# Kernel tuning notes

Hardware: AMD Instinct MI355X
Metric: run time of the kernel (lower is better)

Reference implementation:

```python
import jax, jax.numpy as jnp
import numpy as np
from jax import lax

ALPHA = 0.2
BETA = 10.0
HALF = 1
ITERS = 10


def _slrelu(x):
    return ALPHA * x + (1.0 - ALPHA) * jax.nn.softplus(BETA * x) / BETA


def _std_kernel(sigma):
    # sigma: [C,1,1] -> per-channel L1-normalized Gaussian [C,1,K,K]
    C = sigma.shape[0]
    k = 2 * HALF + 1
    xs = jnp.arange(-HALF, HALF + 1, dtype=jnp.float32)
    r2 = xs[None, :] ** 2 + xs[:, None] ** 2            # [K,K]
    s = jnp.clip(sigma.reshape(C, 1, 1, 1), 1e-6, None)  # [C,1,1,1]
    ker = jnp.exp(-r2[None, None] / (2.0 * s ** 2))      # [C,1,K,K]
    return ker / (jnp.sum(ker, axis=(2, 3), keepdims=True) + 1e-12)


def _dwconv(x, ker):
    # depthwise conv, NCHW input, OIHW kernel [C,1,K,K], groups=C
    C = ker.shape[0]
    return lax.conv_general_dilated(
        x, ker, window_strides=(1, 1), padding=[(HALF, HALF), (HALF, HALF)],
        dimension_numbers=("NCHW", "OIHW", "NCHW"), feature_group_count=C)


def setup_inputs() -> dict:
    key = jax.random.key(0)
    k1, = jax.random.split(key, 1)
    o = jax.random.normal(k1, (8, 64, 256, 256), dtype=jnp.float32)
    nb_sigma = jnp.full((64, 1, 1), 5.0, dtype=jnp.float32)
    lam = jnp.ones((1,), dtype=jnp.float32)
    return {"o": o, "nb_sigma": nb_sigma, "lam": lam}


def reference(o, nb_sigma, lam):
    ker = _std_kernel(nb_sigma)
    u = _slrelu(o)
    l = lam[0]
    for _ in range(ITERS):
        q = _dwconv(1.0 - 2.0 * u, ker)
        u = _slrelu(o - l * q)
    return u
```

## Files before the change

kernel.cpp:

```cpp
#include <hip/hip_runtime.h>

typedef float f4 __attribute__((ext_vector_type(4)));

static constexpr int Hh = 256, Ww = 256, HW = Hh * Ww;
static constexpr int PLANES = 512;
static constexpr int STRIPS = 4;
static constexpr int ROWS   = Hh / STRIPS;
static constexpr int DEPTH  = 10;
static constexpr int RB     = 4;
static constexpr int NSTEP  = (ROWS + 2 * DEPTH) / RB;

#if __has_builtin(__builtin_amdgcn_exp2f)
#define EXP2F(x) __builtin_amdgcn_exp2f(x)
#else
#define EXP2F(x) __expf((x) * 0.6931471805599453f)
#endif

static constexpr float LN2 = 0.6931471805599453f;
static constexpr float L2E = 1.4426950408889634f;
static constexpr float AZS = 10.0f * L2E;

static constexpr float A1 = 0.9897f;
static constexpr float A2 = -0.3059f;
static constexpr float TA = -0.12f * LN2;
static constexpr float TB = -0.08f * LN2;
static constexpr float TCA1 = -0.16f * A1;
static constexpr float TCA2 = -0.16f * A2;
static constexpr float UA = 0.06f * LN2;
static constexpr float UB = 0.04f * LN2;
static constexpr float UCA1 = 0.08f * A1;
static constexpr float UCA2 = 0.08f * A2;

__device__ __forceinline__ float tval_s(float Z) {
    float az = fabsf(Z);
    float p  = EXP2F(-az);
    float r  = fmaf(TCA2, p, TCA1);
    float s  = fmaf(r, p, 1.0f);
    return fmaf(TA, Z, fmaf(TB, az, s));
}
__device__ __forceinline__ float uval_s(float Z) {
    float az = fabsf(Z);
    float p  = EXP2F(-az);
    float r  = fmaf(UCA2, p, UCA1);
    float su = r * p;
    return fmaf(UA, Z, fmaf(UB, az, su));
}

#define STEP_BODY(BORDER) do {                                               \
    float og[DEPTH + RB][4];                                                 \
       \
    _Pragma("unroll")                                                        \
    for (int m = 0; m < RB; ++m)                                             \
        { _Pragma("unroll") for (int i = 0; i < 4; ++i) og[DEPTH + m][i] = AZS * pnext[m][i]; } \
        \
    _Pragma("unroll")                                                        \
    for (int t = DEPTH - 1; t >= 0; --t) {                                   \
        int r = yS - DEPTH + t;                                              \
        if (BORDER) r = r < 0 ? 0 : (r > 255 ? 255 : r);                     \
        f4 v = *reinterpret_cast<const f4*>(op_lane + r * Ww);               \
        og[t][0] = v.x; og[t][1] = v.y; og[t][2] = v.z; og[t][3] = v.w;      \
    }                                                                        \
    \
    _Pragma("unroll")                                                        \
    for (int m = 0; m < RB; ++m) {                                           \
        int r = yS + RB + m;                                                 \
        r = r < 0 ? 0 : (r > 255 ? 255 : r);                                 \
        f4 v = *reinterpret_cast<const f4*>(op_lane + r * Ww);               \
        pnext[m][0] = v.x; pnext[m][1] = v.y; pnext[m][2] = v.z; pnext[m][3] = v.w; \
    }                                                                        \
    asm volatile("" ::: "memory");               \
    float tin[RB][4];                                                        \
    _Pragma("unroll")                                                        \
    for (int m = 0; m < RB; ++m) {                                           \
        const bool rv = !BORDER || (unsigned)(yS + m) < 256u;                \
        _Pragma("unroll")                                                    \
        for (int i = 0; i < 4; ++i) {                                        \
            float tv = tval_s(og[DEPTH + m][i]);                             \
            tin[m][i] = rv ? tv : 0.f;                                       \
        }                                                                    \
    }                                                                        \
      \
    _Pragma("unroll")                                                        \
    for (int t = 0; t < DEPTH; ++t)                                          \
        { _Pragma("unroll") for (int i = 0; i < 4; ++i) og[t][i] *= AZS; }   \
    _Pragma("unroll")                                                        \
    for (int k = 1; k <= DEPTH; ++k) {                                       \
        float hn[RB][4];                                                     \
        _Pragma("unroll")                                                    \
        for (int m = 0; m < RB; ++m) {                                       \
            float lft = __int_as_float(__builtin_amdgcn_ds_bpermute(a_up, __float_as_int(tin[m][3]))); \
            float rgt = __int_as_float(__builtin_amdgcn_ds_bpermute(a_dn, __float_as_int(tin[m][0]))); \
            hn[m][0] = fmaf(w1s, tin[m][0], fmaf(w0s, tin[m][1], w0L * lft)); \
            hn[m][1] = fmaf(w1s, tin[m][1], w0s * (tin[m][0] + tin[m][2]));  \
            hn[m][2] = fmaf(w1s, tin[m][2], w0s * (tin[m][1] + tin[m][3]));  \
            hn[m][3] = fmaf(w1s, tin[m][3], fmaf(w0s, tin[m][2], w0R * rgt)); \
        }                                                                    \
        _Pragma("unroll")                                                    \
        for (int m = 0; m < RB; ++m) {                                       \
            const bool rv = !BORDER || (unsigned)(yS - k + m) < 256u;        \
            _Pragma("unroll")                                                \
            for (int i = 0; i < 4; ++i) {                                    \
                float h_im1 = (m == 0) ? hA[k - 1][i] : (m == 1) ? hB[k - 1][i] : hn[m - 2][i]; \
                float h_i   = (m == 0) ? hB[k - 1][i] : hn[m - 1][i];        \
                float Z = fmaf(W0Z, h_im1 + hn[m][i],                        \
                          fmaf(W1Z, h_i, og[DEPTH - k + m][i]));             \
                if (k < DEPTH) { float tv = tval_s(Z); tin[m][i] = rv ? tv : 0.f; } \
                else           { tin[m][i] = uval_s(Z); }                    \
            }                                                                \
        }                                                                    \
        _Pragma("unroll")                                                    \
        for (int i = 0; i < 4; ++i) { hA[k - 1][i] = hn[2][i]; hB[k - 1][i] = hn[3][i]; } \
    }                                                                        \
    _Pragma("unroll")                                                        \
    for (int m = 0; m < RB; ++m) {                                           \
        const int r = yS - DEPTH + m;                                        \
        if (r >= y0 && r < y0 + ROWS) {                                      \
            f4 v; v.x = tin[m][0]; v.y = tin[m][1]; v.z = tin[m][2]; v.w = tin[m][3]; \
            *reinterpret_cast<f4*>(up_lane + r * Ww) = v;                    \
        }                                                                    \
    }                                                                        \
} while (0)

__global__ __launch_bounds__(64)
__attribute__((amdgpu_waves_per_eu(2, 2)))
void k_fused(const float* __restrict__ o, const float* __restrict__ sigma,
             const float* __restrict__ lam, float* __restrict__ out) {
    const int lane  = threadIdx.x;
    const int bid   = blockIdx.x;
    const int plane = bid >> 2;
    const int strip = bid & 3;
    const int y0    = strip * ROWS;
    const int ch    = plane & 63;

    float s   = fmaxf(sigma[ch], 1e-6f);
    float eg  = __expf(-1.0f / (2.0f * s * s));
    float inv = 1.0f / (1.0f + 2.0f * eg);
    const float w0s = eg * inv, w1s = inv, l = lam[0];
    const float W0Z = -l * w0s * AZS;
    const float W1Z = -l * w1s * AZS;
    const float w0L = (lane == 0)  ? 0.f : w0s;
    const float w0R = (lane == 63) ? 0.f : w0s;

    const float* op_lane = o   + plane * HW + lane * 4;
    float*       up_lane = out + plane * HW + lane * 4;
    const int a_up = ((lane + 63) & 63) << 2;
    const int a_dn = ((lane + 1)  & 63) << 2;

    float hA[DEPTH][4], hB[DEPTH][4];
#pragma unroll
    for (int k = 0; k < DEPTH; ++k)
#pragma unroll
        for (int i = 0; i < 4; ++i) { hA[k][i] = 0.f; hB[k][i] = 0.f; }

    float pnext[RB][4];
#pragma unroll
    for (int m = 0; m < RB; ++m) {
        int r = y0 - DEPTH + m;
        r = r < 0 ? 0 : (r > 255 ? 255 : r);
        f4 v = *reinterpret_cast<const f4*>(op_lane + r * Ww);
        pnext[m][0] = v.x; pnext[m][1] = v.y; pnext[m][2] = v.z; pnext[m][3] = v.w;
    }

    int jb0 = (20 - y0 + 3) / 4; if (jb0 < 0) jb0 = 0;
    int jb1 = (262 - y0) / 4 + 1; if (jb1 > NSTEP) jb1 = NSTEP;

    int j = 0;
#pragma unroll 1
    for (; j < jb0; ++j)  { const int yS = y0 - DEPTH + RB * j; STEP_BODY(true);  }
#pragma unroll 1
    for (; j < jb1; ++j)  { const int yS = y0 - DEPTH + RB * j; STEP_BODY(false); }
#pragma unroll 1
    for (; j < NSTEP; ++j){ const int yS = y0 - DEPTH + RB * j; STEP_BODY(true);  }
}

extern "C" void kernel_launch(void* const* d_in, const int* in_sizes, int n_in,
                              void* d_out, int out_size, void* d_ws, size_t ws_size,
                              hipStream_t stream) {
    (void)in_sizes; (void)n_in; (void)out_size; (void)d_ws; (void)ws_size;
    const float* o     = (const float*)d_in[0];
    const float* sigma = (const float*)d_in[1];
    const float* lam   = (const float*)d_in[2];
    float* out = (float*)d_out;

    k_fused<<<PLANES * STRIPS, 64, 0, stream>>>(o, sigma, lam, out);
}
```

Before: 152.5 us.

## Process two planes per wavefront to interleave independent dependency chains

Each wavefront now handles two planes (p and p+256, same channel) and interleaves their per-depth stages, so the cross-lane permutes of one plane overlap with the arithmetic of the other. This is meant to hide ds_bpermute latency and the serial dependency chain through the ten fused iterations. The grid is halved and waves_per_eu is relaxed to 1-2, which roughly doubles register demand and may lower occupancy or cause spills.

```diff
diff --git a/kernel.cpp b/kernel.cpp
--- a/kernel.cpp
+++ b/kernel.cpp
@@ -20,16 +20,16 @@
 static constexpr float L2E = 1.4426950408889634f;
 static constexpr float AZS = 10.0f * L2E;
 
-static constexpr float A1 = 0.9897f;
-static constexpr float A2 = -0.3059f;
+static constexpr float A1c = 0.9897f;
+static constexpr float A2c = -0.3059f;
 static constexpr float TA = -0.12f * LN2;
 static constexpr float TB = -0.08f * LN2;
-static constexpr float TCA1 = -0.16f * A1;
-static constexpr float TCA2 = -0.16f * A2;
+static constexpr float TCA1 = -0.16f * A1c;
+static constexpr float TCA2 = -0.16f * A2c;
 static constexpr float UA = 0.06f * LN2;
 static constexpr float UB = 0.04f * LN2;
-static constexpr float UCA1 = 0.08f * A1;
-static constexpr float UCA2 = 0.08f * A2;
+static constexpr float UCA1 = 0.08f * A1c;
+static constexpr float UCA2 = 0.08f * A2c;
 
 __device__ __forceinline__ float tval_s(float Z) {
     float az = fabsf(Z);
@@ -46,91 +46,111 @@
     return fmaf(UA, Z, fmaf(UB, az, su));
 }
 
-#define STEP_BODY(BORDER) do {                                               \
-    float og[DEPTH + RB][4];                                                 \
-       \
-    _Pragma("unroll")                                                        \
-    for (int m = 0; m < RB; ++m)                                             \
-        { _Pragma("unroll") for (int i = 0; i < 4; ++i) og[DEPTH + m][i] = AZS * pnext[m][i]; } \
-        \
-    _Pragma("unroll")                                                        \
-    for (int t = DEPTH - 1; t >= 0; --t) {                                   \
+#define CONSUME_PN(S)                                                        \
+    _Pragma("unroll") for (int m = 0; m < RB; ++m)                           \
+    { _Pragma("unroll") for (int i = 0; i < 4; ++i)                          \
+        og##S[DEPTH + m][i] = AZS * pn##S[m][i]; }
+
+#define LOADC(S, BORDER)                                                     \
+    _Pragma("unroll") for (int t = DEPTH - 1; t >= 0; --t) {                 \
         int r = yS - DEPTH + t;                                              \
         if (BORDER) r = r < 0 ? 0 : (r > 255 ? 255 : r);                     \
-        f4 v = *reinterpret_cast<const f4*>(op_lane + r * Ww);               \
-        og[t][0] = v.x; og[t][1] = v.y; og[t][2] = v.z; og[t][3] = v.w;      \
-    }                                                                        \
-    \
-    _Pragma("unroll")                                                        \
-    for (int m = 0; m < RB; ++m) {                                           \
-        int r = yS + RB + m;                                                 \
-        r = r < 0 ? 0 : (r > 255 ? 255 : r);                                 \
-        f4 v = *reinterpret_cast<const f4*>(op_lane + r * Ww);               \
-        pnext[m][0] = v.x; pnext[m][1] = v.y; pnext[m][2] = v.z; pnext[m][3] = v.w; \
-    }                                                                        \
-    asm volatile("" ::: "memory");               \
-    float tin[RB][4];                                                        \
-    _Pragma("unroll")                                                        \
-    for (int m = 0; m < RB; ++m) {                                           \
+        f4 v = *reinterpret_cast<const f4*>(op##S + r * Ww);                 \
+        og##S[t][0]=v.x; og##S[t][1]=v.y; og##S[t][2]=v.z; og##S[t][3]=v.w;  \
+    }
+
+#define PREF(S)                                                              \
+    _Pragma("unroll") for (int m = 0; m < RB; ++m) {                         \
+        int r = yS + RB + m; r = r < 0 ? 0 : (r > 255 ? 255 : r);            \
+        f4 v = *reinterpret_cast<const f4*>(op##S + r * Ww);                 \
+        pn##S[m][0]=v.x; pn##S[m][1]=v.y; pn##S[m][2]=v.z; pn##S[m][3]=v.w;  \
+    }
+
+#define STAGE0(S, BORDER)                                                    \
+    _Pragma("unroll") for (int m = 0; m < RB; ++m) {                         \
         const bool rv = !BORDER || (unsigned)(yS + m) < 256u;                \
-        _Pragma("unroll")                                                    \
-        for (int i = 0; i < 4; ++i) {                                        \
-            float tv = tval_s(og[DEPTH + m][i]);                             \
-            tin[m][i] = rv ? tv : 0.f;                                       \
+        _Pragma("unroll") for (int i = 0; i < 4; ++i) {                      \
+            float tv = tval_s(og##S[DEPTH + m][i]);                          \
+            tin##S[m][i] = rv ? tv : 0.f;                                    \
+        }                                                                    \
+    }
+
+#define SCALEOG(S)                                                           \
+    _Pragma("unroll") for (int t = 0; t < DEPTH; ++t)                        \
+    { _Pragma("unroll") for (int i = 0; i < 4; ++i) og##S[t][i] *= AZS; }
+
+#define PERM(S)                                                              \
+    _Pragma("unroll") for (int m = 0; m < RB; ++m) {                         \
+        lf##S[m] = __int_as_float(__builtin_amdgcn_ds_bpermute(a_up, __float_as_int(tin##S[m][3]))); \
+        rg##S[m] = __int_as_float(__builtin_amdgcn_ds_bpermute(a_dn, __float_as_int(tin##S[m][0]))); \
+    }
+
+#define HFMA(S)                                                              \
+    _Pragma("unroll") for (int m = 0; m < RB; ++m) {                         \
+        hn##S[m][0] = fmaf(w1s, tin##S[m][0], fmaf(w0s, tin##S[m][1], w0L * lf##S[m])); \
+        hn##S[m][1] = fmaf(w1s, tin##S[m][1], w0s * (tin##S[m][0] + tin##S[m][2]));     \
+        hn##S[m][2] = fmaf(w1s, tin##S[m][2], w0s * (tin##S[m][1] + tin##S[m][3]));     \
+        hn##S[m][3] = fmaf(w1s, tin##S[m][3], fmaf(w0s, tin##S[m][2], w0R * rg##S[m])); \
+    }
+
+#define EVALS(S, BORDER)                                                     \
+    _Pragma("unroll") for (int m = 0; m < RB; ++m) {                         \
+        const bool rv = !BORDER || (unsigned)(yS - k + m) < 256u;            \
+        _Pragma("unroll") for (int i = 0; i < 4; ++i) {                      \
+            float h_im1 = (m == 0) ? hA##S[k-1][i] : (m == 1) ? hB##S[k-1][i] : hn##S[m-2][i]; \
+            float h_i   = (m == 0) ? hB##S[k-1][i] : hn##S[m-1][i];          \
+            float Z = fmaf(W0Z, h_im1 + hn##S[m][i],                         \
+                      fmaf(W1Z, h_i, og##S[DEPTH - k + m][i]));              \
+            if (k < DEPTH) { float tv = tval_s(Z); tin##S[m][i] = rv ? tv : 0.f; } \
+            else           { tin##S[m][i] = uval_s(Z); }                     \
         }                                                                    \
     }                                                                        \
-      \
-    _Pragma("unroll")                                                        \
-    for (int t = 0; t < DEPTH; ++t)                                          \
-        { _Pragma("unroll") for (int i = 0; i < 4; ++i) og[t][i] *= AZS; }   \
+    _Pragma("unroll") for (int i = 0; i < 4; ++i) {                          \
+        hA##S[k-1][i] = hn##S[2][i]; hB##S[k-1][i] = hn##S[3][i];            \
+    }
+
+#define STORE(S)                                                             \
+    _Pragma("unroll") for (int m = 0; m < RB; ++m) {                         \
+        const int r = yS - DEPTH + m;                                        \
+        if (r >= y0 && r < y0 + ROWS) {                                      \
+            f4 v; v.x=tin##S[m][0]; v.y=tin##S[m][1]; v.z=tin##S[m][2]; v.w=tin##S[m][3]; \
+            *reinterpret_cast<f4*>(up##S + r * Ww) = v;                      \
+        }                                                                    \
+    }
+
+#define STEP2(BORDER) do {                                                   \
+    float ogA[DEPTH+RB][4], ogB[DEPTH+RB][4];                                \
+    float tinA[RB][4], tinB[RB][4];                                          \
+    float hnA[RB][4],  hnB[RB][4];                                           \
+    float lfA[RB], rgA[RB], lfB[RB], rgB[RB];                                \
+    CONSUME_PN(A) CONSUME_PN(B)                                              \
+    LOADC(A, BORDER) LOADC(B, BORDER)                                        \
+    PREF(A) PREF(B)                                                          \
+    asm volatile("" ::: "memory");                                           \
+    STAGE0(A, BORDER) STAGE0(B, BORDER)                                      \
+    SCALEOG(A) SCALEOG(B)                                                    \
+    PERM(A) PERM(B)                                                          \
     _Pragma("unroll")                                                        \
     for (int k = 1; k <= DEPTH; ++k) {                                       \
-        float hn[RB][4];                                                     \
-        _Pragma("unroll")                                                    \
-        for (int m = 0; m < RB; ++m) {                                       \
-            float lft = __int_as_float(__builtin_amdgcn_ds_bpermute(a_up, __float_as_int(tin[m][3]))); \
-            float rgt = __int_as_float(__builtin_amdgcn_ds_bpermute(a_dn, __float_as_int(tin[m][0]))); \
-            hn[m][0] = fmaf(w1s, tin[m][0], fmaf(w0s, tin[m][1], w0L * lft)); \
-            hn[m][1] = fmaf(w1s, tin[m][1], w0s * (tin[m][0] + tin[m][2]));  \
-            hn[m][2] = fmaf(w1s, tin[m][2], w0s * (tin[m][1] + tin[m][3]));  \
-            hn[m][3] = fmaf(w1s, tin[m][3], fmaf(w0s, tin[m][2], w0R * rgt)); \
-        }                                                                    \
-        _Pragma("unroll")                                                    \
-        for (int m = 0; m < RB; ++m) {                                       \
-            const bool rv = !BORDER || (unsigned)(yS - k + m) < 256u;        \
-            _Pragma("unroll")                                                \
-            for (int i = 0; i < 4; ++i) {                                    \
-                float h_im1 = (m == 0) ? hA[k - 1][i] : (m == 1) ? hB[k - 1][i] : hn[m - 2][i]; \
-                float h_i   = (m == 0) ? hB[k - 1][i] : hn[m - 1][i];        \
-                float Z = fmaf(W0Z, h_im1 + hn[m][i],                        \
-                          fmaf(W1Z, h_i, og[DEPTH - k + m][i]));             \
-                if (k < DEPTH) { float tv = tval_s(Z); tin[m][i] = rv ? tv : 0.f; } \
-                else           { tin[m][i] = uval_s(Z); }                    \
-            }                                                                \
-        }                                                                    \
-        _Pragma("unroll")                                                    \
-        for (int i = 0; i < 4; ++i) { hA[k - 1][i] = hn[2][i]; hB[k - 1][i] = hn[3][i]; } \
+        HFMA(A) EVALS(A, BORDER)                                             \
+        if (k < DEPTH) { PERM(A) }                                           \
+        HFMA(B) EVALS(B, BORDER)                                             \
+        if (k < DEPTH) { PERM(B) }                                           \
     }                                                                        \
-    _Pragma("unroll")                                                        \
-    for (int m = 0; m < RB; ++m) {                                           \
-        const int r = yS - DEPTH + m;                                        \
-        if (r >= y0 && r < y0 + ROWS) {                                      \
-            f4 v; v.x = tin[m][0]; v.y = tin[m][1]; v.z = tin[m][2]; v.w = tin[m][3]; \
-            *reinterpret_cast<f4*>(up_lane + r * Ww) = v;                    \
-        }                                                                    \
-    }                                                                        \
+    STORE(A) STORE(B)                                                        \
 } while (0)
 
 __global__ __launch_bounds__(64)
-__attribute__((amdgpu_waves_per_eu(2, 2)))
+__attribute__((amdgpu_waves_per_eu(1, 2)))
 void k_fused(const float* __restrict__ o, const float* __restrict__ sigma,
              const float* __restrict__ lam, float* __restrict__ out) {
-    const int lane  = threadIdx.x;
-    const int bid   = blockIdx.x;
-    const int plane = bid >> 2;
-    const int strip = bid & 3;
-    const int y0    = strip * ROWS;
-    const int ch    = plane & 63;
+    const int lane   = threadIdx.x;
+    const int bid    = blockIdx.x;
+    const int planeA = bid >> 2;
+    const int planeB = planeA + 256;
+    const int strip  = bid & 3;
+    const int y0     = strip * ROWS;
+    const int ch     = planeA & 63;
 
     float s   = fmaxf(sigma[ch], 1e-6f);
     float eg  = __expf(-1.0f / (2.0f * s * s));
@@ -141,24 +161,31 @@
     const float w0L = (lane == 0)  ? 0.f : w0s;
     const float w0R = (lane == 63) ? 0.f : w0s;
 
-    const float* op_lane = o   + plane * HW + lane * 4;
-    float*       up_lane = out + plane * HW + lane * 4;
+    const float* opA = o   + planeA * HW + lane * 4;
+    const float* opB = o   + planeB * HW + lane * 4;
+    float*       upA = out + planeA * HW + lane * 4;
+    float*       upB = out + planeB * HW + lane * 4;
     const int a_up = ((lane + 63) & 63) << 2;
     const int a_dn = ((lane + 1)  & 63) << 2;
 
-    float hA[DEPTH][4], hB[DEPTH][4];
+    float hAA[DEPTH][4], hBA[DEPTH][4], hAB[DEPTH][4], hBB[DEPTH][4];
 #pragma unroll
     for (int k = 0; k < DEPTH; ++k)
 #pragma unroll
-        for (int i = 0; i < 4; ++i) { hA[k][i] = 0.f; hB[k][i] = 0.f; }
-
-    float pnext[RB][4];
+        for (int i = 0; i < 4; ++i) {
+            hAA[k][i] = 0.f; hBA[k][i] = 0.f;
+            hAB[k][i] = 0.f; hBB[k][i] = 0.f;
+        }
+
+    float pnA[RB][4], pnB[RB][4];
 #pragma unroll
     for (int m = 0; m < RB; ++m) {
         int r = y0 - DEPTH + m;
         r = r < 0 ? 0 : (r > 255 ? 255 : r);
-        f4 v = *reinterpret_cast<const f4*>(op_lane + r * Ww);
-        pnext[m][0] = v.x; pnext[m][1] = v.y; pnext[m][2] = v.z; pnext[m][3] = v.w;
+        f4 va = *reinterpret_cast<const f4*>(opA + r * Ww);
+        f4 vb = *reinterpret_cast<const f4*>(opB + r * Ww);
+        pnA[m][0]=va.x; pnA[m][1]=va.y; pnA[m][2]=va.z; pnA[m][3]=va.w;
+        pnB[m][0]=vb.x; pnB[m][1]=vb.y; pnB[m][2]=vb.z; pnB[m][3]=vb.w;
     }
 
     int jb0 = (20 - y0 + 3) / 4; if (jb0 < 0) jb0 = 0;
@@ -166,11 +193,11 @@
 
     int j = 0;
 #pragma unroll 1
-    for (; j < jb0; ++j)  { const int yS = y0 - DEPTH + RB * j; STEP_BODY(true);  }
+    for (; j < jb0; ++j)  { const int yS = y0 - DEPTH + RB * j; STEP2(true);  }
 #pragma unroll 1
-    for (; j < jb1; ++j)  { const int yS = y0 - DEPTH + RB * j; STEP_BODY(false); }
+    for (; j < jb1; ++j)  { const int yS = y0 - DEPTH + RB * j; STEP2(false); }
 #pragma unroll 1
-    for (; j < NSTEP; ++j){ const int yS = y0 - DEPTH + RB * j; STEP_BODY(true);  }
+    for (; j < NSTEP; ++j){ const int yS = y0 - DEPTH + RB * j; STEP2(true);  }
 }
 
 extern "C" void kernel_launch(void* const* d_in, const int* in_sizes, int n_in,
@@ -182,5 +209,5 @@
     const float* lam   = (const float*)d_in[2];
     float* out = (float*)d_out;
 
-    k_fused<<<PLANES * STRIPS, 64, 0, stream>>>(o, sigma, lam, out);
-}
+    k_fused<<<PLANES * STRIPS / 2, 64, 0, stream>>>(o, sigma, lam, out);
+}
```

New measurement: 186.9 us. 1.23x slower.
